# Kernel tuning notes

Hardware: AMD Instinct MI355X
Metric: run time of the kernel (lower is better)

The kernel has to match this reference:

```python
import jax, jax.numpy as jnp
import numpy as np

N_QUBITS = 12
DIM = 2 ** N_QUBITS  # 4096

_H = (jnp.array([[1.0, 1.0], [1.0, -1.0]]) / np.sqrt(2.0)).astype(jnp.complex64)
_X = jnp.array([[0.0, 1.0], [1.0, 0.0]], dtype=jnp.complex64)


def setup_inputs() -> dict:
    key = jax.random.key(0)
    k1, k2 = jax.random.split(key)
    state = jax.random.normal(k1, (8, 512, DIM), dtype=jnp.float32)
    params = jax.random.normal(k2, (N_QUBITS,), dtype=jnp.float32)
    return {"state": state, "params": params}


def _to_quantum(x):
    # faithful to _classical_to_quantum_inspired: normalize, phase = acos(|v|), sign * exp(i*phase)
    norms = jnp.linalg.norm(x, axis=-1, keepdims=True)
    v = x / (norms + 1e-8)
    mag = jnp.minimum(jnp.abs(v), 1.0)
    q = (jnp.sign(v) * jnp.exp(1j * jnp.arccos(mag))).astype(jnp.complex64)
    nrm = jnp.sqrt(jnp.sum(q.real ** 2 + q.imag ** 2, axis=-1, keepdims=True))
    return q / nrm.astype(jnp.complex64)


def _axis(q):
    # qubit q = bit q (LSB); tensor axes ordered MSB-first after batch axis 0
    return 1 + (N_QUBITS - 1 - q)


def _apply_1q(full, q, U):
    ax = _axis(q)
    moved = jnp.moveaxis(full, ax, -1)
    out = jnp.einsum('...b,ab->...a', moved, U)
    return jnp.moveaxis(out, -1, ax)


def _apply_ctrl(full, c, t, U):
    # apply U on target qubit t where control qubit c == 1
    axc = _axis(c)
    b0 = jnp.take(full, 0, axis=axc)
    b1 = jnp.take(full, 1, axis=axc)
    axt = _axis(t)
    axt_sub = axt - 1 if axt > axc else axt
    moved = jnp.moveaxis(b1, axt_sub, -1)
    b1n = jnp.moveaxis(jnp.einsum('...b,ab->...a', moved, U), -1, axt_sub)
    return jnp.stack([b0, b1n], axis=axc)


def _rx(theta):
    c = jnp.cos(theta / 2).astype(jnp.complex64)
    s = (-1j * jnp.sin(theta / 2)).astype(jnp.complex64)
    return jnp.stack([jnp.stack([c, s]), jnp.stack([s, c])])


def reference(state, params):
    B, T, D = state.shape
    psi = _to_quantum(state.reshape(B * T, D))  # (N, 2**n) complex64
    full = psi.reshape((B * T,) + (2,) * N_QUBITS)
    for q in range(N_QUBITS):
        full = _apply_1q(full, q, _H)                                  # Hadamard
        full = _apply_ctrl(full, q, (q + 1) % N_QUBITS, _rx(params[q]))  # controlled-RX
        if q < N_QUBITS - 1:
            full = _apply_ctrl(full, q, q + 1, _X)                     # CNOT
    amp = full.reshape(B * T, D)
    probs = amp.real ** 2 + amp.imag ** 2  # measurement probabilities
    return probs.reshape(B, T, D).astype(jnp.float32)
```

## Files before the change

kernel.cpp:

```cpp
#include <hip/hip_runtime.h>

#define NQ  12
#define DIM 4096
#define TPB 256

typedef float v2f __attribute__((ext_vector_type(2)));
typedef float v4f __attribute__((ext_vector_type(4)));


__device__ __forceinline__ float wave_reduce(float v) {
#pragma unroll
    for (int m = 32; m >= 1; m >>= 1) v += __shfl_xor(v, m, 64);
    return v;
}

#define BCAST(v, q) __uint_as_float(__builtin_amdgcn_readlane(__float_as_uint(v), (q)))

__device__ __forceinline__ v2f pk_add(v2f a, v2f b) {
    v2f d;
    asm("v_pk_add_f32 %0, %1, %2" : "=v"(d) : "v"(a), "v"(b));
    return d;
}
__device__ __forceinline__ v2f pk_sub(v2f a, v2f b) {
    v2f d;
    asm("v_pk_add_f32 %0, %1, %2 neg_lo:[0,1] neg_hi:[0,1]"
        : "=v"(d) : "v"(a), "v"(b));
    return d;
}
__device__ __forceinline__ v2f pk_mul(v2f a, v2f b) {
    v2f d;
    asm("v_pk_mul_f32 %0, %1, %2" : "=v"(d) : "v"(a), "v"(b));
    return d;
}
__device__ __forceinline__ v2f pk_mul_swap(v2f a, v2f b) {
    v2f d;
    asm("v_pk_mul_f32 %0, %1, %2 op_sel:[0,1] op_sel_hi:[1,0]"
        : "=v"(d) : "v"(a), "v"(b));
    return d;
}
__device__ __forceinline__ v2f pk_fma(v2f a, v2f b, v2f c) {
    v2f d;
    asm("v_pk_fma_f32 %0, %1, %2, %3" : "=v"(d) : "v"(a), "v"(b), "v"(c));
    return d;
}

template <int MC, int MT, bool XGATE>
__device__ __forceinline__ void apply_layer(v2f* a, v2f ctv, v2f snv) {
#pragma unroll
    for (int i = 0; i < 16; ++i) {
        if (i & MC) continue;
        const int j = i | MC;
        const v2f t0 = a[i], t1 = a[j];
        a[i] = pk_add(t0, t1);
        a[j] = pk_sub(t0, t1);
    }
#pragma unroll
    for (int i = 0; i < 16; ++i) {
        if (!(i & MC) || (i & MT)) continue;
        const int j = i | MT;
        const v2f b0 = a[i], b1 = a[j];
        const v2f s0 = pk_mul_swap(snv, b0);
        const v2f s1 = pk_mul_swap(snv, b1);
        if (XGATE) {
            a[i] = pk_fma(ctv, b1, s0);
            a[j] = pk_fma(ctv, b0, s1);
        } else {
            a[i] = pk_fma(ctv, b0, s1);
            a[j] = pk_fma(ctv, b1, s0);
        }
    }
}

__global__ __launch_bounds__(TPB, 5) void qlayer_kernel(
        const float* __restrict__ state, const float* __restrict__ params,
        float* __restrict__ out) {
    __shared__ __align__(16) v2f amp[DIM];
    char* const lds = (char*)amp;

    const int t = threadIdx.x;
    const int lane = t & 63;
    const long long sbase = (long long)blockIdx.x * DIM;

    const float th = params[lane < NQ ? lane : 0] * 0.5f;
    const float cl = cosf(th);
    const float sl = sinf(th);

    const float4* gp = (const float4*)(state + sbase + t * 16);
    float4 xv[4];
    float ss = 0.f;
#pragma unroll
    for (int j = 0; j < 4; ++j) {
        const float4 v = gp[j];
        xv[j] = v;
        ss = fmaf(v.x, v.x, ss); ss = fmaf(v.y, v.y, ss);
        ss = fmaf(v.z, v.z, ss); ss = fmaf(v.w, v.w, ss);
    }
    ss = wave_reduce(ss);
    if (lane == 0) ((float*)lds)[t >> 6] = ss;
    __syncthreads();
    const float* redp = (const float*)lds;
    const float sst = redp[0] + redp[1] + redp[2] + redp[3];
    const float invd = __builtin_amdgcn_rsqf(sst);
    __syncthreads();

    v2f a[16];
#define ENC(k, xval)                                                      \
    {                                                                     \
        const float v   = (xval) * invd;                                  \
        const float re  = fminf(fmaxf(v, -1.0f), 1.0f);                   \
        const float imb = __builtin_amdgcn_sqrtf(fmaxf(1.0f - re * re, 0.f)); \
        const float im  = (v > 0.f) ? imb : ((v < 0.f) ? -imb : 0.f);     \
        v2f q; q.x = re; q.y = im;                                        \
        a[k] = q;                                                         \
    }
#pragma unroll
    for (int j = 0; j < 4; ++j) {
        const float4 xq = xv[j];
        ENC(4 * j + 0, xq.x); ENC(4 * j + 1, xq.y);
        ENC(4 * j + 2, xq.z); ENC(4 * j + 3, xq.w);
    }
#undef ENC

#define CTV(q) ({ v2f _c; _c.x = BCAST(cl, q); _c.y = _c.x; _c; })
#define SNV(q) ({ float _s = BCAST(sl, q); v2f _v; _v.x = _s; _v.y = -_s; _v; })

    apply_layer<1, 2, true>(a, CTV(0), SNV(0));
    apply_layer<2, 4, true>(a, CTV(1), SNV(1));
    apply_layer<4, 8, true>(a, CTV(2), SNV(2));
    {
        const int v1b = (t << 7) | (((t >> 1) & 7) << 4);
#pragma unroll
        for (int k = 0; k < 8; ++k) {
            v4f w; w.x = a[2 * k].x; w.y = a[2 * k].y;
            w.z = a[2 * k + 1].x; w.w = a[2 * k + 1].y;
            *(v4f*)(lds + (v1b ^ (k << 4))) = w;
        }
    }

    {
        const int g  = t >> 3;
        const int gp2 = g & 1;
        const int baseE = ((t & 7) << 3) + (g << 10) + (gp2 << 6);
        const int baseO = ((t & 7) << 3) + (g << 10) + ((1 - gp2) << 6);
#pragma unroll
        for (int r = 0; r < 16; ++r)
            a[r] = *(const v2f*)(lds +
                ((((r & 1) ? baseO : baseE) ^ ((r >> 2) << 4)) + ((r >> 1) << 7)));
        apply_layer<1, 2, true>(a, CTV(3), SNV(3));
        apply_layer<2, 4, true>(a, CTV(4), SNV(4));
        apply_layer<4, 8, true>(a, CTV(5), SNV(5));
#pragma unroll
        for (int r = 0; r < 16; ++r)
            *(v2f*)(lds +
                ((((r & 1) ? baseO : baseE) ^ ((r >> 2) << 4)) + ((r >> 1) << 7))) = a[r];
    }

    {
        const int b3b = (((t & 63) ^ (((t >> 5) & 1) << 1)) << 3) + ((t >> 6) << 13);
#pragma unroll
        for (int r = 0; r < 16; ++r)
            a[r] = *(const v2f*)(lds + ((b3b ^ ((r & 3) << 5)) + (r << 9)));
        apply_layer<1, 2, true>(a, CTV(6), SNV(6));
        apply_layer<2, 4, true>(a, CTV(7), SNV(7));
        apply_layer<4, 8, true>(a, CTV(8), SNV(8));
#pragma unroll
        for (int r = 0; r < 16; ++r)
            *(v2f*)(lds + ((b3b ^ ((r & 3) << 5)) + (r << 9))) = a[r];
    }
    __syncthreads();

    {
        const int F0b = (t << 4) ^ (((t >> 4) & 7) << 4);
#pragma unroll
        for (int k = 0; k < 8; ++k) {
            const v4f v = *(const v4f*)(lds + (F0b + (k << 12)));
            v2f q0; q0.x = v.x; q0.y = v.y;
            v2f q1; q1.x = v.z; q1.y = v.w;
            a[k] = q0;
            a[k + 8] = q1;
        }
        apply_layer<1, 2, true >(a, CTV(9),  SNV(9));
        apply_layer<2, 4, true >(a, CTV(10), SNV(10));
        apply_layer<4, 8, false>(a, CTV(11), SNV(11));

        v2f sc2; sc2.x = 0x1p-24f; sc2.y = 0x1p-24f;
        v2f* outp = (v2f*)(out + sbase);
#pragma unroll
        for (int k = 0; k < 8; ++k) {
            const v2f q0 = pk_mul(a[k], a[k]);
            const v2f q1 = pk_mul(a[k | 8], a[k | 8]);
            v2f res; res.x = q0.x + q0.y;
            res.y = q1.x + q1.y;
            res = pk_mul(res, sc2);
            __builtin_nontemporal_store(res, outp + t + (k << 8));
        }
    }
#undef CTV
#undef SNV
}

extern "C" void kernel_launch(void* const* d_in, const int* in_sizes, int n_in,
                              void* d_out, int out_size, void* d_ws, size_t ws_size,
                              hipStream_t stream) {
    (void)in_sizes; (void)n_in; (void)out_size; (void)d_ws; (void)ws_size;
    const float* state  = (const float*)d_in[0];
    const float* params = (const float*)d_in[1];
    float* out = (float*)d_out;
    qlayer_kernel<<<dim3(4096), dim3(TPB), 0, stream>>>(state, params, out);
}
```

Before: 115.2 us.

## Halve LDS buffer with two-pass transposes to raise occupancy

Shrinks the shared-memory state buffer from 32KB to 16KB by doing each inter-stage transpose in two half-passes per wave, and raises the launch-bounds occupancy hint from 5 to 8 blocks. The middle transposes are reorganised to stay within each wave's private 4KB slice, so the block-wide barriers around them are removed. The final cross-wave transpose now takes extra barriers and two write/read rounds. Keeping a second register array may raise register pressure under the tighter launch bound.

```diff
diff --git a/kernel.cpp b/kernel.cpp
--- a/kernel.cpp
+++ b/kernel.cpp
@@ -17,31 +17,23 @@
 #define BCAST(v, q) __uint_as_float(__builtin_amdgcn_readlane(__float_as_uint(v), (q)))
 
 __device__ __forceinline__ v2f pk_add(v2f a, v2f b) {
-    v2f d;
-    asm("v_pk_add_f32 %0, %1, %2" : "=v"(d) : "v"(a), "v"(b));
-    return d;
+    v2f d; asm("v_pk_add_f32 %0, %1, %2" : "=v"(d) : "v"(a), "v"(b)); return d;
 }
 __device__ __forceinline__ v2f pk_sub(v2f a, v2f b) {
     v2f d;
-    asm("v_pk_add_f32 %0, %1, %2 neg_lo:[0,1] neg_hi:[0,1]"
-        : "=v"(d) : "v"(a), "v"(b));
+    asm("v_pk_add_f32 %0, %1, %2 neg_lo:[0,1] neg_hi:[0,1]" : "=v"(d) : "v"(a), "v"(b));
     return d;
 }
 __device__ __forceinline__ v2f pk_mul(v2f a, v2f b) {
-    v2f d;
-    asm("v_pk_mul_f32 %0, %1, %2" : "=v"(d) : "v"(a), "v"(b));
-    return d;
+    v2f d; asm("v_pk_mul_f32 %0, %1, %2" : "=v"(d) : "v"(a), "v"(b)); return d;
 }
 __device__ __forceinline__ v2f pk_mul_swap(v2f a, v2f b) {
     v2f d;
-    asm("v_pk_mul_f32 %0, %1, %2 op_sel:[0,1] op_sel_hi:[1,0]"
-        : "=v"(d) : "v"(a), "v"(b));
+    asm("v_pk_mul_f32 %0, %1, %2 op_sel:[0,1] op_sel_hi:[1,0]" : "=v"(d) : "v"(a), "v"(b));
     return d;
 }
 __device__ __forceinline__ v2f pk_fma(v2f a, v2f b, v2f c) {
-    v2f d;
-    asm("v_pk_fma_f32 %0, %1, %2, %3" : "=v"(d) : "v"(a), "v"(b), "v"(c));
-    return d;
+    v2f d; asm("v_pk_fma_f32 %0, %1, %2, %3" : "=v"(d) : "v"(a), "v"(b), "v"(c)); return d;
 }
 
 template <int MC, int MT, bool XGATE>
@@ -61,24 +53,20 @@
         const v2f b0 = a[i], b1 = a[j];
         const v2f s0 = pk_mul_swap(snv, b0);
         const v2f s1 = pk_mul_swap(snv, b1);
-        if (XGATE) {
-            a[i] = pk_fma(ctv, b1, s0);
-            a[j] = pk_fma(ctv, b0, s1);
-        } else {
-            a[i] = pk_fma(ctv, b0, s1);
-            a[j] = pk_fma(ctv, b1, s0);
-        }
-    }
-}
-
-__global__ __launch_bounds__(TPB, 5) void qlayer_kernel(
+        if (XGATE) { a[i] = pk_fma(ctv, b1, s0); a[j] = pk_fma(ctv, b0, s1); }
+        else       { a[i] = pk_fma(ctv, b0, s1); a[j] = pk_fma(ctv, b1, s0); }
+    }
+}
+
+__global__ __launch_bounds__(TPB, 8) void qlayer_kernel(
         const float* __restrict__ state, const float* __restrict__ params,
         float* __restrict__ out) {
-    __shared__ __align__(16) v2f amp[DIM];
-    char* const lds = (char*)amp;
+    __shared__ __align__(16) v2f buf[2048];
+    char* const lds = (char*)buf;
 
     const int t = threadIdx.x;
     const int lane = t & 63;
+    const int wv = t >> 6;
     const long long sbase = (long long)blockIdx.x * DIM;
 
     const float th = params[lane < NQ ? lane : 0] * 0.5f;
@@ -96,12 +84,13 @@
         ss = fmaf(v.z, v.z, ss); ss = fmaf(v.w, v.w, ss);
     }
     ss = wave_reduce(ss);
-    if (lane == 0) ((float*)lds)[t >> 6] = ss;
+    if (lane == 0) {
+#pragma unroll
+        for (int s = 0; s < 4; ++s) *(float*)(lds + (s << 12) + (wv << 2)) = ss;
+    }
     __syncthreads();
-    const float* redp = (const float*)lds;
-    const float sst = redp[0] + redp[1] + redp[2] + redp[3];
-    const float invd = __builtin_amdgcn_rsqf(sst);
-    __syncthreads();
+    const float* pr = (const float*)(lds + (wv << 12));
+    const float invd = __builtin_amdgcn_rsqf(pr[0] + pr[1] + pr[2] + pr[3]);
 
     v2f a[16];
 #define ENC(k, xval)                                                      \
@@ -127,68 +116,106 @@
     apply_layer<1, 2, true>(a, CTV(0), SNV(0));
     apply_layer<2, 4, true>(a, CTV(1), SNV(1));
     apply_layer<4, 8, true>(a, CTV(2), SNV(2));
-    {
-        const int v1b = (t << 7) | (((t >> 1) & 7) << 4);
-#pragma unroll
-        for (int k = 0; k < 8; ++k) {
+
+    v2f b[16];
+    {
+        const int B1w = ((wv << 12) | ((t & 63) << 6)) ^ (((t >> 1) & 3) << 4);
+        const int B1r = (wv << 12) | ((t & 7) << 3) | (((t >> 3) & 7) << 9);
+        const bool hs = ((t >> 2) & 1) != 0;
+#pragma unroll
+        for (int c = 0; c < 2; ++c) {
+            const bool hi = hs ^ (c != 0);
+#pragma unroll
+            for (int k = 0; k < 4; ++k) {
+                const v2f lo = hi ? a[8 + 2 * k] : a[2 * k];
+                const v2f h1 = hi ? a[9 + 2 * k] : a[2 * k + 1];
+                v4f w; w.x = lo.x; w.y = lo.y; w.z = h1.x; w.w = h1.y;
+                *(v4f*)(lds + (B1w ^ (k << 4))) = w;
+            }
+#pragma unroll
+            for (int m = 0; m < 8; ++m) {
+                const int rp = (m << 1) | (c ^ (m >> 2));
+                const int C  = (m << 6) | (((m >> 1) & 3) << 4);
+                b[rp] = *(const v2f*)(lds + (B1r ^ C));
+            }
+        }
+    }
+
+    apply_layer<1, 2, true>(b, CTV(3), SNV(3));
+    apply_layer<2, 4, true>(b, CTV(4), SNV(4));
+    apply_layer<4, 8, true>(b, CTV(5), SNV(5));
+
+    {
+        const int B2w = ((wv << 12) | (((t >> 3) & 7) << 9) | ((t & 7) << 6))
+                        ^ (((t >> 1) & 3) << 4);
+        const int B2r = ((wv << 12) | ((t & 7) << 6) | (((t >> 3) & 7) << 3))
+                        ^ (((t >> 1) & 3) << 4);
+        const bool hs = ((t >> 5) & 1) != 0;
+#pragma unroll
+        for (int c = 0; c < 2; ++c) {
+            const bool hi = hs ^ (c != 0);
+#pragma unroll
+            for (int k = 0; k < 4; ++k) {
+                const v2f lo = hi ? b[8 + 2 * k] : b[2 * k];
+                const v2f h1 = hi ? b[9 + 2 * k] : b[2 * k + 1];
+                v4f w; w.x = lo.x; w.y = lo.y; w.z = h1.x; w.w = h1.y;
+                *(v4f*)(lds + (B2w ^ (k << 4))) = w;
+            }
+#pragma unroll
+            for (int m = 0; m < 8; ++m) {
+                const int rp = (m << 1) | (c ^ (m >> 2));
+                a[rp] = *(const v2f*)(lds + B2r + (m << 9));
+            }
+        }
+    }
+
+    apply_layer<1, 2, true>(a, CTV(6), SNV(6));
+    apply_layer<2, 4, true>(a, CTV(7), SNV(7));
+    apply_layer<4, 8, true>(a, CTV(8), SNV(8));
+
+    {
+        const int B3w = (((t & 63) << 6) | (wv << 12))
+                        ^ (((t >> 1) & 3) << 4) ^ (((t >> 4) & 1) << 6);
+        const int B4r = ((((t >> 5) & 7) << 3) | ((t & 31) << 7))
+                        ^ ((t & 3) << 4) ^ (((t >> 3) & 1) << 6);
+#pragma unroll
+        for (int k = 0; k < 4; ++k) {
             v4f w; w.x = a[2 * k].x; w.y = a[2 * k].y;
             w.z = a[2 * k + 1].x; w.w = a[2 * k + 1].y;
-            *(v4f*)(lds + (v1b ^ (k << 4))) = w;
-        }
-    }
-
-    {
-        const int g  = t >> 3;
-        const int gp2 = g & 1;
-        const int baseE = ((t & 7) << 3) + (g << 10) + (gp2 << 6);
-        const int baseO = ((t & 7) << 3) + (g << 10) + ((1 - gp2) << 6);
-#pragma unroll
-        for (int r = 0; r < 16; ++r)
-            a[r] = *(const v2f*)(lds +
-                ((((r & 1) ? baseO : baseE) ^ ((r >> 2) << 4)) + ((r >> 1) << 7)));
-        apply_layer<1, 2, true>(a, CTV(3), SNV(3));
-        apply_layer<2, 4, true>(a, CTV(4), SNV(4));
-        apply_layer<4, 8, true>(a, CTV(5), SNV(5));
-#pragma unroll
-        for (int r = 0; r < 16; ++r)
-            *(v2f*)(lds +
-                ((((r & 1) ? baseO : baseE) ^ ((r >> 2) << 4)) + ((r >> 1) << 7))) = a[r];
-    }
-
-    {
-        const int b3b = (((t & 63) ^ (((t >> 5) & 1) << 1)) << 3) + ((t >> 6) << 13);
-#pragma unroll
-        for (int r = 0; r < 16; ++r)
-            a[r] = *(const v2f*)(lds + ((b3b ^ ((r & 3) << 5)) + (r << 9)));
-        apply_layer<1, 2, true>(a, CTV(6), SNV(6));
-        apply_layer<2, 4, true>(a, CTV(7), SNV(7));
-        apply_layer<4, 8, true>(a, CTV(8), SNV(8));
-#pragma unroll
-        for (int r = 0; r < 16; ++r)
-            *(v2f*)(lds + ((b3b ^ ((r & 3) << 5)) + (r << 9))) = a[r];
-    }
-    __syncthreads();
-
-    {
-        const int F0b = (t << 4) ^ (((t >> 4) & 7) << 4);
-#pragma unroll
-        for (int k = 0; k < 8; ++k) {
-            const v4f v = *(const v4f*)(lds + (F0b + (k << 12)));
-            v2f q0; q0.x = v.x; q0.y = v.y;
-            v2f q1; q1.x = v.z; q1.y = v.w;
-            a[k] = q0;
-            a[k + 8] = q1;
-        }
-        apply_layer<1, 2, true >(a, CTV(9),  SNV(9));
-        apply_layer<2, 4, true >(a, CTV(10), SNV(10));
-        apply_layer<4, 8, false>(a, CTV(11), SNV(11));
-
+            *(v4f*)(lds + (B3w ^ (k << 4))) = w;
+        }
+        __syncthreads();
+#pragma unroll
+        for (int j = 0; j < 4; ++j) {
+            b[(j << 1)]     = *(const v2f*)(lds + (B4r + (j << 12)));
+            b[(j << 1) | 8] = *(const v2f*)(lds + ((B4r ^ 64) + (j << 12)));
+        }
+        __syncthreads();
+#pragma unroll
+        for (int k = 0; k < 4; ++k) {
+            v4f w; w.x = a[8 + 2 * k].x; w.y = a[8 + 2 * k].y;
+            w.z = a[9 + 2 * k].x; w.w = a[9 + 2 * k].y;
+            *(v4f*)(lds + (B3w ^ (k << 4))) = w;
+        }
+        __syncthreads();
+#pragma unroll
+        for (int j = 0; j < 4; ++j) {
+            b[(j << 1) | 1]     = *(const v2f*)(lds + (B4r + (j << 12)));
+            b[(j << 1) | 1 | 8] = *(const v2f*)(lds + ((B4r ^ 64) + (j << 12)));
+        }
+    }
+
+    apply_layer<1, 2, true >(b, CTV(9),  SNV(9));
+    apply_layer<2, 4, true >(b, CTV(10), SNV(10));
+    apply_layer<4, 8, false>(b, CTV(11), SNV(11));
+
+    {
         v2f sc2; sc2.x = 0x1p-24f; sc2.y = 0x1p-24f;
         v2f* outp = (v2f*)(out + sbase);
 #pragma unroll
         for (int k = 0; k < 8; ++k) {
-            const v2f q0 = pk_mul(a[k], a[k]);
-            const v2f q1 = pk_mul(a[k | 8], a[k | 8]);
+            const v2f q0 = pk_mul(b[k], b[k]);
+            const v2f q1 = pk_mul(b[k | 8], b[k | 8]);
             v2f res; res.x = q0.x + q0.y;
             res.y = q1.x + q1.y;
             res = pk_mul(res, sc2);
```

Result: no change. 116.3 us (+0.9%).
